# Optimization experiments

Hardware: AMD Instinct MI355X
Metric: run time of the kernel (lower is better)

Reference implementation:

```python
import jax, jax.numpy as jnp
import numpy as np

DIM = 64
HEADS = 4
HEAD_DIM = DIM // HEADS
HIDDEN = DIM * 2
B, N = 8, 2048


def _layernorm(x, g, b, eps=1e-5):
    mu = jnp.mean(x, axis=-1, keepdims=True)
    var = jnp.var(x, axis=-1, keepdims=True)
    return (x - mu) * jax.lax.rsqrt(var + eps) * g + b


def setup_inputs() -> dict:
    key = jax.random.key(0)
    ks = jax.random.split(key, 12)
    s = 0.02
    return {
        "x": jax.random.normal(ks[0], (B, N, DIM), jnp.float32),
        "clinic": jax.random.normal(ks[1], (B, N, DIM), jnp.float32),
        "norm1_g": jnp.ones((DIM,), jnp.float32),
        "norm1_b": jnp.zeros((DIM,), jnp.float32),
        "norm2_g": jnp.ones((DIM,), jnp.float32),
        "norm2_b": jnp.zeros((DIM,), jnp.float32),
        "Wkv": jax.random.normal(ks[2], (DIM, 2 * DIM), jnp.float32) * s,
        "bkv": jnp.zeros((2 * DIM,), jnp.float32),
        "Wq": jax.random.normal(ks[3], (DIM, DIM), jnp.float32) * s,
        "bq": jnp.zeros((DIM,), jnp.float32),
        "Wproj": jax.random.normal(ks[4], (DIM, DIM), jnp.float32) * s,
        "bproj": jnp.zeros((DIM,), jnp.float32),
        "W1": jax.random.normal(ks[5], (DIM, HIDDEN), jnp.float32) * s,
        "b1": jnp.zeros((HIDDEN,), jnp.float32),
        "W2": jax.random.normal(ks[6], (HIDDEN, DIM), jnp.float32) * s,
        "b2": jnp.zeros((DIM,), jnp.float32),
    }


def reference(x, clinic, norm1_g, norm1_b, norm2_g, norm2_b,
              Wkv, bkv, Wq, bq, Wproj, bproj, W1, b1, W2, b2):
    # shared norm1 on both streams (as in the torch code)
    xn = _layernorm(x, norm1_g, norm1_b)
    cn = _layernorm(clinic, norm1_g, norm1_b)
    scale = HEAD_DIM ** -0.5
    # K/V from x, Q from clinic
    kv = (xn @ Wkv + bkv).reshape(B, N, 2, HEADS, HEAD_DIM)
    k = kv[:, :, 0].transpose(0, 2, 1, 3)  # [B,H,N,hd]
    v = kv[:, :, 1].transpose(0, 2, 1, 3)
    q = (cn @ Wq + bq).reshape(B, N, HEADS, HEAD_DIM).transpose(0, 2, 1, 3)
    attn = jax.nn.softmax(jnp.einsum('bhqd,bhkd->bhqk', q, k) * scale, axis=-1)
    o = jnp.einsum('bhqk,bhkd->bhqd', attn, v).transpose(0, 2, 1, 3).reshape(B, N, DIM)
    o = o @ Wproj + bproj
    # MLP with residual (dropout/drop_path are inference no-ops)
    h = _layernorm(o, norm2_g, norm2_b)
    h = jax.nn.gelu(h @ W1 + b1, approximate=False) @ W2 + b2
    return o + h
```

## Files before the change

kernel.cpp:

```cpp
#include <hip/hip_runtime.h>
#include <hip/hip_bf16.h>
#include <math.h>

#define B_    8
#define N_    2048
#define DIM_  64
#define H_    4
#define HD_   16
#define HID_  128
#define NROWS (B_ * N_)
#define KVB   64
#define QSCALE (0.25f * 1.4426950408889634f)

typedef float    f32x4 __attribute__((ext_vector_type(4)));
typedef __fp16   hfx2  __attribute__((ext_vector_type(2)));
typedef _Float16 f16x4 __attribute__((ext_vector_type(4)));
typedef _Float16 f16x8 __attribute__((ext_vector_type(8)));

#define MFMA16(a, b, c) __builtin_amdgcn_mfma_f32_16x16x16f16((a), (b), (c), 0, 0, 0)

__device__ __forceinline__ float ex2(float x) {
#if __has_builtin(__builtin_amdgcn_exp2f)
    return __builtin_amdgcn_exp2f(x);
#else
    return exp2f(x);
#endif
}

__global__ __launch_bounds__(256) void k1_ln_qkv(
    const float* __restrict__ x, const float* __restrict__ clinic,
    const float* __restrict__ n1g, const float* __restrict__ n1b,
    const float* __restrict__ Wkv, const float* __restrict__ bkv,
    const float* __restrict__ Wq,  const float* __restrict__ bq,
    _Float16* __restrict__ Kd, _Float16* __restrict__ Vd,
    _Float16* __restrict__ Qd)
{
    __shared__ _Float16 WkvT[128][68];
    __shared__ _Float16 WqT [64][68];
    __shared__ _Float16 xnT [64][68];
    __shared__ _Float16 cnT [64][68];

    const int tid  = threadIdx.x;
    const int row0 = blockIdx.x * 64;

    for (int i = tid; i < 64 * 128; i += 256) {
        const int d = i >> 7, c = i & 127;
        WkvT[c][d] = (_Float16)Wkv[i];
    }
    for (int i = tid; i < 64 * 64; i += 256) {
        const int d = i >> 6, c = i & 63;
        WqT[c][d] = (_Float16)Wq[i];
    }

    {
        const int r = tid >> 4, s = tid & 15;
        const float4 gv = *(const float4*)(n1g + s * 4);
        const float4 bv = *(const float4*)(n1b + s * 4);
        #pragma unroll
        for (int it = 0; it < 4; ++it) {
            const int rl = it * 16 + r;
            const int rg = row0 + rl;
            float4 xv = *(const float4*)(x      + (size_t)rg * DIM_ + s * 4);
            float4 cv = *(const float4*)(clinic + (size_t)rg * DIM_ + s * 4);

            float xs = xv.x + xv.y + xv.z + xv.w;
            float cs = cv.x + cv.y + cv.z + cv.w;
            #pragma unroll
            for (int m = 1; m < 16; m <<= 1) {
                xs += __shfl_xor(xs, m);
                cs += __shfl_xor(cs, m);
            }
            const float xmu = xs * (1.f / 64.f);
            const float cmu = cs * (1.f / 64.f);
            float4 xd = make_float4(xv.x - xmu, xv.y - xmu, xv.z - xmu, xv.w - xmu);
            float4 cd = make_float4(cv.x - cmu, cv.y - cmu, cv.z - cmu, cv.w - cmu);

            float xq = xd.x * xd.x + xd.y * xd.y + xd.z * xd.z + xd.w * xd.w;
            float cq = cd.x * cd.x + cd.y * cd.y + cd.z * cd.z + cd.w * cd.w;
            #pragma unroll
            for (int m = 1; m < 16; m <<= 1) {
                xq += __shfl_xor(xq, m);
                cq += __shfl_xor(cq, m);
            }
            const float xinv = rsqrtf(xq * (1.f / 64.f) + 1e-5f);
            const float cinv = rsqrtf(cq * (1.f / 64.f) + 1e-5f);

            xnT[rl][s * 4 + 0] = (_Float16)(xd.x * xinv * gv.x + bv.x);
            xnT[rl][s * 4 + 1] = (_Float16)(xd.y * xinv * gv.y + bv.y);
            xnT[rl][s * 4 + 2] = (_Float16)(xd.z * xinv * gv.z + bv.z);
            xnT[rl][s * 4 + 3] = (_Float16)(xd.w * xinv * gv.w + bv.w);
            cnT[rl][s * 4 + 0] = (_Float16)(cd.x * cinv * gv.x + bv.x);
            cnT[rl][s * 4 + 1] = (_Float16)(cd.y * cinv * gv.y + bv.y);
            cnT[rl][s * 4 + 2] = (_Float16)(cd.z * cinv * gv.z + bv.z);
            cnT[rl][s * 4 + 3] = (_Float16)(cd.w * cinv * gv.w + bv.w);
        }
    }
    __syncthreads();

    const int lane = tid & 63, wave = tid >> 6;
    const int col  = lane & 15;
    const int grp4 = (lane >> 4) * 4;
    const int arow = wave * 16 + col;
    const f32x4 Z = {0.f, 0.f, 0.f, 0.f};

    f16x4 ax[4], ac[4];
    #pragma unroll
    for (int kt = 0; kt < 4; ++kt) {
        ax[kt] = *(const f16x4*)&xnT[arow][kt * 16 + grp4];
        ac[kt] = *(const f16x4*)&cnT[arow][kt * 16 + grp4];
    }

    #pragma unroll
    for (int ct = 0; ct < 8; ++ct) {
        f32x4 acc = Z;
        #pragma unroll
        for (int kt = 0; kt < 4; ++kt) {
            const f16x4 bf = *(const f16x4*)&WkvT[ct * 16 + col][kt * 16 + grp4];
            acc = MFMA16(ax[kt], bf, acc);
        }
        const int c = ct * 16 + col;
        const float bias = bkv[c];
        _Float16* dst = (c & 64) ? Vd : Kd;
        const int hh = (c >> 4) & 3, dd = c & 15;
        #pragma unroll
        for (int r = 0; r < 4; ++r) {
            const int rg = row0 + wave * 16 + grp4 + r;
            const int b = rg >> 11, n = rg & (N_ - 1);
            dst[(((size_t)(b * H_ + hh)) * N_ + n) * HD_ + dd] =
                (_Float16)(acc[r] + bias);
        }
    }
    #pragma unroll
    for (int ct = 0; ct < 4; ++ct) {
        f32x4 acc = Z;
        #pragma unroll
        for (int kt = 0; kt < 4; ++kt) {
            const f16x4 bf = *(const f16x4*)&WqT[ct * 16 + col][kt * 16 + grp4];
            acc = MFMA16(ac[kt], bf, acc);
        }
        const int c = ct * 16 + col;
        const float bias = bq[c];
        const int hh = c >> 4, dd = c & 15;
        #pragma unroll
        for (int r = 0; r < 4; ++r) {
            const int rg = row0 + wave * 16 + grp4 + r;
            const int b = rg >> 11, n = rg & (N_ - 1);
            Qd[(((size_t)(b * H_ + hh)) * N_ + n) * HD_ + dd] =
                (_Float16)((acc[r] + bias) * QSCALE);
        }
    }
}

__global__ __launch_bounds__(256, 4) void k2_attn(
    const _Float16* __restrict__ Kd, const _Float16* __restrict__ Vd,
    const _Float16* __restrict__ Qd, float* __restrict__ O)
{
    __shared__ _Float16 Vt[4][2][16][68];

    const int tid  = threadIdx.x;
    const int lane = tid & 63;
    const int wave = tid >> 6;
    const int col  = lane & 15;
    const int grp  = lane >> 4;
    const int grp4 = grp * 4;

    const int wg = (blockIdx.x & 7) * 256 + (blockIdx.x >> 3);
    const int bh = wg >> 6;
    const int qt = wg & 63;

    const _Float16* Kbh = Kd + (size_t)bh * (N_ * HD_);
    const _Float16* Vbh = Vd + (size_t)bh * (N_ * HD_);
    const _Float16* Qbh = Qd + (size_t)bh * (N_ * HD_);

    const int qbase = qt * 32;
    const f16x4 qf0 = *(const f16x4*)(Qbh + (qbase + col) * HD_ + grp4);
    const f16x4 qf1 = *(const f16x4*)(Qbh + (qbase + 16 + col) * HD_ + grp4);

    const int k0   = wave * 512;
    const int koff = (k0 + col) * HD_ + grp4;
    const int voff = (k0 + lane) * HD_;

    float l0 = 0.f, l1 = 0.f;
    f32x4 o0 = {0.f, 0.f, 0.f, 0.f};
    f32x4 o1 = {0.f, 0.f, 0.f, 0.f};

    f16x4 kf[4];
    #pragma unroll
    for (int sb = 0; sb < 4; ++sb)
        kf[sb] = *(const f16x4*)(Kbh + koff + sb * (16 * HD_));
    {
        const f16x8 va = *(const f16x8*)(Vbh + voff);
        const f16x8 vb = *(const f16x8*)(Vbh + voff + 8);
        #pragma unroll
        for (int hh = 0; hh < 8; ++hh) {
            Vt[wave][0][hh][lane]     = va[hh];
            Vt[wave][0][hh + 8][lane] = vb[hh];
        }
    }

    int cur = 0;
    for (int kt = 0; kt < 8; ++kt) {
        const int nxo = ((kt + 1) & 7) * (KVB * HD_);
        f16x4 kn[4];
        #pragma unroll
        for (int sb = 0; sb < 4; ++sb)
            kn[sb] = *(const f16x4*)(Kbh + koff + nxo + sb * (16 * HD_));
        const f16x8 vna = *(const f16x8*)(Vbh + voff + nxo);
        const f16x8 vnb = *(const f16x8*)(Vbh + voff + nxo + 8);

        const f32x4 Z = {0.f, 0.f, 0.f, 0.f};
        f32x4 s0[4], s1[4];
        #pragma unroll
        for (int sb = 0; sb < 4; ++sb) {
            s0[sb] = MFMA16(kf[sb], qf0, Z);
            s1[sb] = MFMA16(kf[sb], qf1, Z);
        }

        f16x4 vf[4];
        #pragma unroll
        for (int sb = 0; sb < 4; ++sb)
            vf[sb] = *(const f16x4*)&Vt[wave][cur][col][sb * 16 + grp4];

        f16x4 pf0[4], pf1[4];
        #pragma unroll
        for (int sb = 0; sb < 4; ++sb) {
            const float a0 = ex2(s0[sb][0]), a1 = ex2(s0[sb][1]);
            const float a2 = ex2(s0[sb][2]), a3 = ex2(s0[sb][3]);
            l0 += (a0 + a1) + (a2 + a3);
            const hfx2 lo = __builtin_amdgcn_cvt_pkrtz(a0, a1);
            const hfx2 hi = __builtin_amdgcn_cvt_pkrtz(a2, a3);
            pf0[sb] = (f16x4){(_Float16)lo[0], (_Float16)lo[1],
                              (_Float16)hi[0], (_Float16)hi[1]};
            const float b0 = ex2(s1[sb][0]), b1 = ex2(s1[sb][1]);
            const float b2 = ex2(s1[sb][2]), b3 = ex2(s1[sb][3]);
            l1 += (b0 + b1) + (b2 + b3);
            const hfx2 lo1 = __builtin_amdgcn_cvt_pkrtz(b0, b1);
            const hfx2 hi1 = __builtin_amdgcn_cvt_pkrtz(b2, b3);
            pf1[sb] = (f16x4){(_Float16)lo1[0], (_Float16)lo1[1],
                              (_Float16)hi1[0], (_Float16)hi1[1]};
        }

        #pragma unroll
        for (int sb = 0; sb < 4; ++sb) {
            o0 = MFMA16(pf0[sb], vf[sb], o0);
            o1 = MFMA16(pf1[sb], vf[sb], o1);
        }

        #pragma unroll
        for (int hh = 0; hh < 8; ++hh) {
            Vt[wave][cur ^ 1][hh][lane]     = vna[hh];
            Vt[wave][cur ^ 1][hh + 8][lane] = vnb[hh];
        }
        kf[0] = kn[0]; kf[1] = kn[1]; kf[2] = kn[2]; kf[3] = kn[3];
        cur ^= 1;
    }

    l0 += __shfl_xor(l0, 16); l0 += __shfl_xor(l0, 32);
    l1 += __shfl_xor(l1, 16); l1 += __shfl_xor(l1, 32);

    __syncthreads();
    float* smP = (float*)&Vt[0][0][0][0];
    float* smL = smP + 4 * 32 * 17;
    #pragma unroll
    for (int r = 0; r < 4; ++r) {
        smP[(wave * 32 + grp4 + r) * 17 + col]      = o0[r];
        smP[(wave * 32 + 16 + grp4 + r) * 17 + col] = o1[r];
    }
    if (grp == 0) {
        smL[wave * 32 + col]      = l0;
        smL[wave * 32 + 16 + col] = l1;
    }
    __syncthreads();

    {
        const int q = tid >> 3, hp = (tid & 7) * 2;
        const float ls = smL[q] + smL[32 + q] + smL[64 + q] + smL[96 + q];
        const float rl = 1.f / ls;
        float v0 = 0.f, v1 = 0.f;
        #pragma unroll
        for (int w = 0; w < 4; ++w) {
            v0 += smP[(w * 32 + q) * 17 + hp];
            v1 += smP[(w * 32 + q) * 17 + hp + 1];
        }
        const int b = bh >> 2, h = bh & 3;
        float* dst = O + ((size_t)b * N_ + qbase + q) * DIM_ + h * HD_ + hp;
        dst[0] = v0 * rl;
        dst[1] = v1 * rl;
    }
}

__device__ __forceinline__ float gelu_fast(float v) {
    const float t = v * v;
    const float z = v * fmaf(0.035677408f, t, 0.79788456f);
    const float e = ex2(z * 2.8853900817779268f);
    const float r = __builtin_amdgcn_rcpf(e + 1.0f);
    return v * e * r;
}

__global__ __launch_bounds__(256) void k3_proj_mlp(
    const float* __restrict__ O,
    const float* __restrict__ Wproj, const float* __restrict__ bproj,
    const float* __restrict__ n2g,   const float* __restrict__ n2b,
    const float* __restrict__ W1,    const float* __restrict__ b1,
    const float* __restrict__ W2,    const float* __restrict__ b2,
    float* __restrict__ out)
{
    __shared__ _Float16 WpT [64][68];
    __shared__ _Float16 W1T [128][68];
    __shared__ _Float16 W2T [64][136];
    __shared__ _Float16 aT  [64][68];
    __shared__ float    sp  [64][68];
    __shared__ _Float16 hT  [64][68];
    __shared__ _Float16 actT[64][136];

    const int tid  = threadIdx.x;
    const int row0 = blockIdx.x * 64;

    for (int i = tid; i < 64 * 64; i += 256) {
        const int k = i >> 6, c = i & 63;
        WpT[c][k] = (_Float16)Wproj[i];
    }
    for (int i = tid; i < 64 * 128; i += 256) {
        const int k = i >> 7, c = i & 127;
        W1T[c][k] = (_Float16)W1[i];
    }
    for (int i = tid; i < 128 * 64; i += 256) {
        const int k = i >> 6, c = i & 63;
        W2T[c][k] = (_Float16)W2[i];
    }
    {
        const int r = tid >> 2, c0 = (tid & 3) * 16;
        const float4* src = (const float4*)(O + (size_t)(row0 + r) * DIM_ + c0);
        #pragma unroll
        for (int j = 0; j < 4; ++j) {
            const float4 v = src[j];
            aT[r][c0 + j * 4 + 0] = (_Float16)v.x;
            aT[r][c0 + j * 4 + 1] = (_Float16)v.y;
            aT[r][c0 + j * 4 + 2] = (_Float16)v.z;
            aT[r][c0 + j * 4 + 3] = (_Float16)v.w;
        }
    }
    __syncthreads();

    const int lane = tid & 63, wave = tid >> 6;
    const int col  = lane & 15;
    const int grp4 = (lane >> 4) * 4;
    const int arow = wave * 16 + col;
    const f32x4 Z = {0.f, 0.f, 0.f, 0.f};

    {
        f16x4 af[4];
        #pragma unroll
        for (int kt = 0; kt < 4; ++kt)
            af[kt] = *(const f16x4*)&aT[arow][kt * 16 + grp4];
        #pragma unroll
        for (int ct = 0; ct < 4; ++ct) {
            f32x4 acc = Z;
            #pragma unroll
            for (int kt = 0; kt < 4; ++kt) {
                const f16x4 bf = *(const f16x4*)&WpT[ct * 16 + col][kt * 16 + grp4];
                acc = MFMA16(af[kt], bf, acc);
            }
            const int c = ct * 16 + col;
            const float bias = bproj[c];
            #pragma unroll
            for (int r = 0; r < 4; ++r)
                sp[wave * 16 + grp4 + r][c] = acc[r] + bias;
        }
    }
    __syncthreads();

    {
        const int r = tid >> 4, s = tid & 15;
        const float4 gv = *(const float4*)(n2g + s * 4);
        const float4 bv = *(const float4*)(n2b + s * 4);
        #pragma unroll
        for (int it = 0; it < 4; ++it) {
            const int rl = it * 16 + r;
            const float4 v = *(const float4*)&sp[rl][s * 4];
            float sm = v.x + v.y + v.z + v.w;
            #pragma unroll
            for (int m = 1; m < 16; m <<= 1) sm += __shfl_xor(sm, m);
            const float mu = sm * (1.f / 64.f);
            float4 d4 = make_float4(v.x - mu, v.y - mu, v.z - mu, v.w - mu);
            float qs = d4.x * d4.x + d4.y * d4.y + d4.z * d4.z + d4.w * d4.w;
            #pragma unroll
            for (int m = 1; m < 16; m <<= 1) qs += __shfl_xor(qs, m);
            const float inv = rsqrtf(qs * (1.f / 64.f) + 1e-5f);
            hT[rl][s * 4 + 0] = (_Float16)(d4.x * inv * gv.x + bv.x);
            hT[rl][s * 4 + 1] = (_Float16)(d4.y * inv * gv.y + bv.y);
            hT[rl][s * 4 + 2] = (_Float16)(d4.z * inv * gv.z + bv.z);
            hT[rl][s * 4 + 3] = (_Float16)(d4.w * inv * gv.w + bv.w);
        }
    }
    __syncthreads();

    {
        f16x4 hf[4];
        #pragma unroll
        for (int kt = 0; kt < 4; ++kt)
            hf[kt] = *(const f16x4*)&hT[arow][kt * 16 + grp4];
        #pragma unroll
        for (int ct = 0; ct < 8; ++ct) {
            f32x4 acc = Z;
            #pragma unroll
            for (int kt = 0; kt < 4; ++kt) {
                const f16x4 bf = *(const f16x4*)&W1T[ct * 16 + col][kt * 16 + grp4];
                acc = MFMA16(hf[kt], bf, acc);
            }
            const int c = ct * 16 + col;
            const float bias = b1[c];
            #pragma unroll
            for (int r = 0; r < 4; ++r)
                actT[wave * 16 + grp4 + r][c] =
                    (_Float16)gelu_fast(acc[r] + bias);
        }
    }

    {
        f16x4 pf[8];
        #pragma unroll
        for (int kt = 0; kt < 8; ++kt)
            pf[kt] = *(const f16x4*)&actT[arow][kt * 16 + grp4];
        #pragma unroll
        for (int ct = 0; ct < 4; ++ct) {
            f32x4 acc = Z;
            #pragma unroll
            for (int kt = 0; kt < 8; ++kt) {
                const f16x4 bf = *(const f16x4*)&W2T[ct * 16 + col][kt * 16 + grp4];
                acc = MFMA16(pf[kt], bf, acc);
            }
            const int c = ct * 16 + col;
            const float bias = b2[c];
            #pragma unroll
            for (int r = 0; r < 4; ++r) {
                const int rl = wave * 16 + grp4 + r;
                out[(size_t)(row0 + rl) * DIM_ + c] = acc[r] + bias + sp[rl][c];
            }
        }
    }
}

extern "C" void kernel_launch(void* const* d_in, const int* in_sizes, int n_in,
                              void* d_out, int out_size, void* d_ws, size_t ws_size,
                              hipStream_t stream) {
    const float* x      = (const float*)d_in[0];
    const float* clinic = (const float*)d_in[1];
    const float* n1g    = (const float*)d_in[2];
    const float* n1b    = (const float*)d_in[3];
    const float* n2g    = (const float*)d_in[4];
    const float* n2b    = (const float*)d_in[5];
    const float* Wkv    = (const float*)d_in[6];
    const float* bkv    = (const float*)d_in[7];
    const float* Wq     = (const float*)d_in[8];
    const float* bq     = (const float*)d_in[9];
    const float* Wproj  = (const float*)d_in[10];
    const float* bproj  = (const float*)d_in[11];
    const float* W1     = (const float*)d_in[12];
    const float* b1     = (const float*)d_in[13];
    const float* W2     = (const float*)d_in[14];
    const float* b2     = (const float*)d_in[15];
    float* out = (float*)d_out;

    char* ws = (char*)d_ws;
    const size_t SZ = (size_t)B_ * H_ * N_ * HD_;
    _Float16* Kd = (_Float16*)ws;
    _Float16* Vd = (_Float16*)(ws + 2 * SZ);
    _Float16* Qd = (_Float16*)(ws + 4 * SZ);
    float*    O  = (float*)   (ws + 6 * SZ);

    k1_ln_qkv<<<NROWS / 64, 256, 0, stream>>>(x, clinic, n1g, n1b, Wkv, bkv,
                                              Wq, bq, Kd, Vd, Qd);
    k2_attn<<<32 * 64, 256, 0, stream>>>(Kd, Vd, Qd, O);
    k3_proj_mlp<<<NROWS / 64, 256, 0, stream>>>(O, Wproj, bproj, n2g, n2b,
                                                W1, b1, W2, b2, out);
}
```

Measured before the change: 43.28 us.

## Double attention query tile to 64 rows per block to reuse K/V

Each attention workgroup now handles 64 queries instead of 32, with four query sub-tiles sharing each K fragment and transposed V tile loaded per key block. This halves the grid and the global K/V traffic and LDS V-transposes per query. The epilogue now merges through a union LDS buffer and writes float4 stores. The cost is more accumulator registers per thread, fewer blocks, and a lowered occupancy hint in launch bounds.

```diff
diff --git a/kernel.cpp b/kernel.cpp
--- a/kernel.cpp
+++ b/kernel.cpp
@@ -151,38 +151,42 @@
     }
 }
 
-__global__ __launch_bounds__(256, 4) void k2_attn(
+__global__ __launch_bounds__(256, 3) void k2_attn(
     const _Float16* __restrict__ Kd, const _Float16* __restrict__ Vd,
     const _Float16* __restrict__ Qd, float* __restrict__ O)
 {
-    __shared__ _Float16 Vt[4][2][16][68];
+    __shared__ union {
+        _Float16 vt[4][2][16][70];
+        float    mg[4][64][18];
+    } sm;
+    __shared__ float smL[4][64];
 
     const int tid  = threadIdx.x;
     const int lane = tid & 63;
     const int wave = tid >> 6;
     const int col  = lane & 15;
-    const int grp  = lane >> 4;
-    const int grp4 = grp * 4;
-
-    const int wg = (blockIdx.x & 7) * 256 + (blockIdx.x >> 3);
-    const int bh = wg >> 6;
-    const int qt = wg & 63;
+    const int grp4 = (lane >> 4) * 4;
+
+    const int wg = (blockIdx.x & 7) * 128 + (blockIdx.x >> 3);
+    const int bh = wg >> 5;
+    const int qt = wg & 31;
 
     const _Float16* Kbh = Kd + (size_t)bh * (N_ * HD_);
     const _Float16* Vbh = Vd + (size_t)bh * (N_ * HD_);
     const _Float16* Qbh = Qd + (size_t)bh * (N_ * HD_);
 
-    const int qbase = qt * 32;
-    const f16x4 qf0 = *(const f16x4*)(Qbh + (qbase + col) * HD_ + grp4);
-    const f16x4 qf1 = *(const f16x4*)(Qbh + (qbase + 16 + col) * HD_ + grp4);
+    const int qbase = qt * 64;
+    f16x4 qf[4];
+    #pragma unroll
+    for (int qp = 0; qp < 4; ++qp)
+        qf[qp] = *(const f16x4*)(Qbh + (qbase + qp * 16 + col) * HD_ + grp4);
 
     const int k0   = wave * 512;
     const int koff = (k0 + col) * HD_ + grp4;
     const int voff = (k0 + lane) * HD_;
 
-    float l0 = 0.f, l1 = 0.f;
-    f32x4 o0 = {0.f, 0.f, 0.f, 0.f};
-    f32x4 o1 = {0.f, 0.f, 0.f, 0.f};
+    float l0 = 0.f, l1 = 0.f, l2 = 0.f, l3 = 0.f;
+    f32x4 o0 = {0.f, 0.f, 0.f, 0.f}, o1 = o0, o2 = o0, o3 = o0;
 
     f16x4 kf[4];
     #pragma unroll
@@ -193,8 +197,8 @@
         const f16x8 vb = *(const f16x8*)(Vbh + voff + 8);
         #pragma unroll
         for (int hh = 0; hh < 8; ++hh) {
-            Vt[wave][0][hh][lane]     = va[hh];
-            Vt[wave][0][hh + 8][lane] = vb[hh];
+            sm.vt[wave][0][hh][lane]     = va[hh];
+            sm.vt[wave][0][hh + 8][lane] = vb[hh];
         }
     }
 
@@ -208,48 +212,46 @@
         const f16x8 vna = *(const f16x8*)(Vbh + voff + nxo);
         const f16x8 vnb = *(const f16x8*)(Vbh + voff + nxo + 8);
 
+        f16x4 vf[4];
+        #pragma unroll
+        for (int sb = 0; sb < 4; ++sb)
+            vf[sb] = *(const f16x4*)&sm.vt[wave][cur][col][sb * 16 + grp4];
+
         const f32x4 Z = {0.f, 0.f, 0.f, 0.f};
-        f32x4 s0[4], s1[4];
-        #pragma unroll
-        for (int sb = 0; sb < 4; ++sb) {
-            s0[sb] = MFMA16(kf[sb], qf0, Z);
-            s1[sb] = MFMA16(kf[sb], qf1, Z);
-        }
-
-        f16x4 vf[4];
-        #pragma unroll
-        for (int sb = 0; sb < 4; ++sb)
-            vf[sb] = *(const f16x4*)&Vt[wave][cur][col][sb * 16 + grp4];
-
-        f16x4 pf0[4], pf1[4];
-        #pragma unroll
-        for (int sb = 0; sb < 4; ++sb) {
-            const float a0 = ex2(s0[sb][0]), a1 = ex2(s0[sb][1]);
-            const float a2 = ex2(s0[sb][2]), a3 = ex2(s0[sb][3]);
-            l0 += (a0 + a1) + (a2 + a3);
-            const hfx2 lo = __builtin_amdgcn_cvt_pkrtz(a0, a1);
-            const hfx2 hi = __builtin_amdgcn_cvt_pkrtz(a2, a3);
-            pf0[sb] = (f16x4){(_Float16)lo[0], (_Float16)lo[1],
-                              (_Float16)hi[0], (_Float16)hi[1]};
-            const float b0 = ex2(s1[sb][0]), b1 = ex2(s1[sb][1]);
-            const float b2 = ex2(s1[sb][2]), b3 = ex2(s1[sb][3]);
-            l1 += (b0 + b1) + (b2 + b3);
-            const hfx2 lo1 = __builtin_amdgcn_cvt_pkrtz(b0, b1);
-            const hfx2 hi1 = __builtin_amdgcn_cvt_pkrtz(b2, b3);
-            pf1[sb] = (f16x4){(_Float16)lo1[0], (_Float16)lo1[1],
-                              (_Float16)hi1[0], (_Float16)hi1[1]};
-        }
-
-        #pragma unroll
-        for (int sb = 0; sb < 4; ++sb) {
-            o0 = MFMA16(pf0[sb], vf[sb], o0);
-            o1 = MFMA16(pf1[sb], vf[sb], o1);
+        #pragma unroll
+        for (int qp = 0; qp < 4; ++qp) {
+            f32x4 s[4];
+            #pragma unroll
+            for (int sb = 0; sb < 4; ++sb)
+                s[sb] = MFMA16(kf[sb], qf[qp], Z);
+
+            float pl = 0.f;
+            f16x4 pf[4];
+            #pragma unroll
+            for (int sb = 0; sb < 4; ++sb) {
+                const float a0 = ex2(s[sb][0]), a1 = ex2(s[sb][1]);
+                const float a2 = ex2(s[sb][2]), a3 = ex2(s[sb][3]);
+                pl += (a0 + a1) + (a2 + a3);
+                const hfx2 lo = __builtin_amdgcn_cvt_pkrtz(a0, a1);
+                const hfx2 hi = __builtin_amdgcn_cvt_pkrtz(a2, a3);
+                pf[sb] = (f16x4){(_Float16)lo[0], (_Float16)lo[1],
+                                 (_Float16)hi[0], (_Float16)hi[1]};
+            }
+            if (qp == 0) { l0 += pl; }
+            else if (qp == 1) { l1 += pl; }
+            else if (qp == 2) { l2 += pl; }
+            else { l3 += pl; }
+
+            f32x4& o = (qp == 0) ? o0 : (qp == 1) ? o1 : (qp == 2) ? o2 : o3;
+            #pragma unroll
+            for (int sb = 0; sb < 4; ++sb)
+                o = MFMA16(pf[sb], vf[sb], o);
         }
 
         #pragma unroll
         for (int hh = 0; hh < 8; ++hh) {
-            Vt[wave][cur ^ 1][hh][lane]     = vna[hh];
-            Vt[wave][cur ^ 1][hh + 8][lane] = vnb[hh];
+            sm.vt[wave][cur ^ 1][hh][lane]     = vna[hh];
+            sm.vt[wave][cur ^ 1][hh + 8][lane] = vnb[hh];
         }
         kf[0] = kn[0]; kf[1] = kn[1]; kf[2] = kn[2]; kf[3] = kn[3];
         cur ^= 1;
@@ -257,35 +259,37 @@
 
     l0 += __shfl_xor(l0, 16); l0 += __shfl_xor(l0, 32);
     l1 += __shfl_xor(l1, 16); l1 += __shfl_xor(l1, 32);
-
-    __syncthreads();
-    float* smP = (float*)&Vt[0][0][0][0];
-    float* smL = smP + 4 * 32 * 17;
+    l2 += __shfl_xor(l2, 16); l2 += __shfl_xor(l2, 32);
+    l3 += __shfl_xor(l3, 16); l3 += __shfl_xor(l3, 32);
+
+    __syncthreads();
     #pragma unroll
     for (int r = 0; r < 4; ++r) {
-        smP[(wave * 32 + grp4 + r) * 17 + col]      = o0[r];
-        smP[(wave * 32 + 16 + grp4 + r) * 17 + col] = o1[r];
-    }
-    if (grp == 0) {
-        smL[wave * 32 + col]      = l0;
-        smL[wave * 32 + 16 + col] = l1;
-    }
-    __syncthreads();
-
-    {
-        const int q = tid >> 3, hp = (tid & 7) * 2;
-        const float ls = smL[q] + smL[32 + q] + smL[64 + q] + smL[96 + q];
+        sm.mg[wave][ 0 + grp4 + r][col] = o0[r];
+        sm.mg[wave][16 + grp4 + r][col] = o1[r];
+        sm.mg[wave][32 + grp4 + r][col] = o2[r];
+        sm.mg[wave][48 + grp4 + r][col] = o3[r];
+    }
+    if ((lane >> 4) == 0) {
+        smL[wave][ 0 + col] = l0;
+        smL[wave][16 + col] = l1;
+        smL[wave][32 + col] = l2;
+        smL[wave][48 + col] = l3;
+    }
+    __syncthreads();
+
+    {
+        const int q = tid >> 2, h4 = (tid & 3) * 4;
+        const float ls = smL[0][q] + smL[1][q] + smL[2][q] + smL[3][q];
         const float rl = 1.f / ls;
-        float v0 = 0.f, v1 = 0.f;
-        #pragma unroll
-        for (int w = 0; w < 4; ++w) {
-            v0 += smP[(w * 32 + q) * 17 + hp];
-            v1 += smP[(w * 32 + q) * 17 + hp + 1];
-        }
+        float v[4];
+        #pragma unroll
+        for (int j = 0; j < 4; ++j)
+            v[j] = (sm.mg[0][q][h4 + j] + sm.mg[1][q][h4 + j] +
+                    sm.mg[2][q][h4 + j] + sm.mg[3][q][h4 + j]) * rl;
         const int b = bh >> 2, h = bh & 3;
-        float* dst = O + ((size_t)b * N_ + qbase + q) * DIM_ + h * HD_ + hp;
-        dst[0] = v0 * rl;
-        dst[1] = v1 * rl;
+        float* dst = O + ((size_t)b * N_ + qbase + q) * DIM_ + h * HD_ + h4;
+        *(float4*)dst = make_float4(v[0], v[1], v[2], v[3]);
     }
 }
 
@@ -471,7 +475,7 @@
 
     k1_ln_qkv<<<NROWS / 64, 256, 0, stream>>>(x, clinic, n1g, n1b, Wkv, bkv,
                                               Wq, bq, Kd, Vd, Qd);
-    k2_attn<<<32 * 64, 256, 0, stream>>>(Kd, Vd, Qd, O);
+    k2_attn<<<32 * 32, 256, 0, stream>>>(Kd, Vd, Qd, O);
     k3_proj_mlp<<<NROWS / 64, 256, 0, stream>>>(O, Wproj, bproj, n2g, n2b,
                                                 W1, b1, W2, b2, out);
 }
```

Result: no change. 42.94 us (-0.8%).
